# Kernel tuning notes

Hardware: AMD Instinct MI355X
Metric: run time of the kernel (lower is better)

Reference implementation:

```python
import jax, jax.numpy as jnp
import numpy as np

N_NODES = 100000
N_EDGES = 1600000
D_FEAT = 64
POS_DIM = 3
D_HID = 64


def setup_inputs() -> dict:
    key = jax.random.key(0)
    ks = jax.random.split(key, 8)
    s = lambda fan_in: 1.0 / np.sqrt(fan_in)
    x = jax.random.normal(ks[0], (N_NODES, D_FEAT), dtype=jnp.float32)
    pos = jax.random.normal(ks[1], (N_NODES, POS_DIM), dtype=jnp.float32)
    edge_index = jax.random.randint(ks[2], (2, N_EDGES), 0, N_NODES, dtype=jnp.int64)
    d_msg_in = 2 * D_FEAT + POS_DIM  # 131
    d_agg_in = 2 * D_FEAT            # 128
    return {
        "x": x,
        "edge_index": edge_index,
        "pos": pos,
        "mw1": jax.random.normal(ks[3], (d_msg_in, D_HID), dtype=jnp.float32) * s(d_msg_in),
        "mb1": jnp.zeros((D_HID,), dtype=jnp.float32),
        "mw2": jax.random.normal(ks[4], (D_HID, D_HID), dtype=jnp.float32) * s(D_HID),
        "mb2": jnp.zeros((D_HID,), dtype=jnp.float32),
        "aw1": jax.random.normal(ks[5], (d_agg_in, D_HID), dtype=jnp.float32) * s(d_agg_in),
        "ab1": jnp.zeros((D_HID,), dtype=jnp.float32),
        "aw2": jax.random.normal(ks[6], (D_HID, D_HID), dtype=jnp.float32) * s(D_HID),
        "ab2": jnp.zeros((D_HID,), dtype=jnp.float32),
    }


def reference(x, edge_index, pos, mw1, mb1, mw2, mb2, aw1, ab1, aw2, ab2):
    # flow='target_to_source': aggregation node i = edge_index[0], neighbor j = edge_index[1]
    i = edge_index[0]
    j = edge_index[1]
    # message: msg_net(cat[x_i, x_j, pos_j - pos_i])   [E, 2d+pos]
    inp = jnp.concatenate([x[i], x[j], pos[j] - pos[i]], axis=1)
    h = jax.nn.relu(inp @ mw1 + mb1)
    msg = h @ mw2 + mb2  # [E, D_HID]
    n = x.shape[0]
    # scatter-mean aggregate at node i
    msg_sum = jax.ops.segment_sum(msg, i, num_segments=n)
    cnt = jax.ops.segment_sum(jnp.ones((i.shape[0], 1), x.dtype), i, num_segments=n)
    aggr = msg_sum / jnp.maximum(cnt, 1.0)
    # update: aggr_net(cat[x, aggr])  (self_val=True)
    u = jnp.concatenate([x, aggr], axis=1)
    return jax.nn.relu(u @ aw1 + ab1) @ aw2 + ab2
```

## Files before the change

kernel.cpp:

```cpp
#include <hip/hip_runtime.h>
#include <hip/hip_fp16.h>

#define N_NODES 100000
#define N_EDGES 1600000
#define NPART 98
#define CAP   20480
#define EB    8192
#define NBB   ((N_EDGES + EB - 1) / EB)
#define NBT   ((N_NODES + 127) / 128)

typedef _Float16 half8 __attribute__((ext_vector_type(8)));
typedef float f32x4 __attribute__((ext_vector_type(4)));

#define WS_OFF   0
#define WS_PCUR  400016
#define WS_B     400528
#define WS_SJ    401040
#define WS_BCOMB 6817424
#define WS_PK    6817680
#define WS_Q     6858640
#define WS_BIN   19658640
#define WS_HM16  19658640

__global__ void __launch_bounds__(256) k_setup(const float* __restrict__ mw1,
                                               const float* __restrict__ mw2,
                                               const float* __restrict__ mb2,
                                               const float* __restrict__ aw1,
                                               const float* __restrict__ aw2,
                                               _Float16* __restrict__ pk,
                                               float* __restrict__ bcomb,
                                               int* __restrict__ pcur) {
    __shared__ float wc[4096];
    int blk = blockIdx.x, t = threadIdx.x;
    if (blk < 5) {
        const float* src;
        if (blk == 3) {
            for (int o = t; o < 4096; o += 256) {
                int c = o >> 6, k = o & 63;
                float s = 0.f;
                #pragma unroll 8
                for (int a = 0; a < 64; ++a) s += mw2[c * 64 + a] * aw1[(64 + a) * 64 + k];
                wc[o] = s;
            }
            __syncthreads();
            src = wc;
        } else {
            src = (blk == 0) ? mw1 : (blk == 1) ? (mw1 + 4096)
                : (blk == 2) ? aw1 : aw2;
        }
        _Float16* dst = pk + blk * 4096;
        for (int o = t; o < 4096; o += 256) {
            int b_ = o & 7, l = (o >> 3) & 63, z = o >> 9;
            int kg = z & 1, nt = z >> 1;
            int k = kg * 32 + ((l >> 4) << 3) + b_;
            int n = nt * 16 + (l & 15);
            dst[o] = (_Float16)src[k * 64 + n];
        }
    } else {
        if (t < 64) {
            float s = 0.f;
            #pragma unroll 8
            for (int a = 0; a < 64; ++a) s += mb2[a] * aw1[(64 + a) * 64 + t];
            bcomb[t] = s;
        }
        if (t < 128) pcur[t] = t * CAP;
    }
}

__device__ __forceinline__ half8 afrag_f32(const float* src, int row, int kg, int l) {
    const float* p = src + (size_t)row * 64 + kg * 32 + ((l >> 4) << 3);
    float4 u = *(const float4*)p;
    float4 v = *(const float4*)(p + 4);
    half8 h;
    h[0] = (_Float16)u.x; h[1] = (_Float16)u.y; h[2] = (_Float16)u.z; h[3] = (_Float16)u.w;
    h[4] = (_Float16)v.x; h[5] = (_Float16)v.y; h[6] = (_Float16)v.z; h[7] = (_Float16)v.w;
    return h;
}

__global__ void __launch_bounds__(256) k_binpre(const int* __restrict__ ei,
                                                const int* __restrict__ ej,
                                                int* pcur, int* __restrict__ binned,
                                                const float* __restrict__ x,
                                                const float* __restrict__ pos,
                                                const float* __restrict__ mw1,
                                                const float* __restrict__ mb1,
                                                const _Float16* __restrict__ pk,
                                                float* __restrict__ P,
                                                _Float16* __restrict__ Q16) {
    __shared__ int cnt[NPART];
    __shared__ int wcur[NPART];
    int t = threadIdx.x;
    if (blockIdx.x < NBB) {
        for (int q = t; q < NPART; q += 256) cnt[q] = 0;
        __syncthreads();
        int base_e = blockIdx.x * EB;
        #pragma unroll 2
        for (int it = 0; it < EB / 1024; ++it) {
            int e = base_e + it * 1024 + t * 4;
            if (e < N_EDGES) {
                int4 iv = *(const int4*)(ei + e);
                atomicAdd(&cnt[iv.x >> 10], 1);
                atomicAdd(&cnt[iv.y >> 10], 1);
                atomicAdd(&cnt[iv.z >> 10], 1);
                atomicAdd(&cnt[iv.w >> 10], 1);
            }
        }
        __syncthreads();
        for (int q = t; q < NPART; q += 256)
            wcur[q] = cnt[q] ? atomicAdd(&pcur[q], cnt[q]) : 0;
        __syncthreads();
        #pragma unroll 2
        for (int it = 0; it < EB / 1024; ++it) {
            int e = base_e + it * 1024 + t * 4;
            if (e < N_EDGES) {
                int4 iv = *(const int4*)(ei + e);
                int4 jv = *(const int4*)(ej + e);
                int a, p;
                p = iv.x >> 10; a = atomicAdd(&wcur[p], 1);
                if (a < (p + 1) * CAP) binned[a] = ((iv.x & 1023) << 17) | jv.x;
                p = iv.y >> 10; a = atomicAdd(&wcur[p], 1);
                if (a < (p + 1) * CAP) binned[a] = ((iv.y & 1023) << 17) | jv.y;
                p = iv.z >> 10; a = atomicAdd(&wcur[p], 1);
                if (a < (p + 1) * CAP) binned[a] = ((iv.z & 1023) << 17) | jv.z;
                p = iv.w >> 10; a = atomicAdd(&wcur[p], 1);
                if (a < (p + 1) * CAP) binned[a] = ((iv.w & 1023) << 17) | jv.w;
            }
        }
        return;
    }
    int bid = blockIdx.x - NBB;
    int w = t >> 6, l = t & 63;
    int m0 = bid * 128 + w * 32;

    half8 a[2][2];
    #pragma unroll
    for (int s = 0; s < 2; ++s)
        #pragma unroll
        for (int kg = 0; kg < 2; ++kg) {
            int row = m0 + s * 16 + (l & 15);
            if (row >= N_NODES) row = N_NODES - 1;
            a[s][kg] = afrag_f32(x, row, kg, l);
        }

    f32x4 z = {0.f, 0.f, 0.f, 0.f};
    f32x4 accP[2][4], accQ[2][4];
    #pragma unroll
    for (int s = 0; s < 2; ++s)
        #pragma unroll
        for (int nt = 0; nt < 4; ++nt) { accP[s][nt] = z; accQ[s][nt] = z; }

    #pragma unroll
    for (int nt = 0; nt < 4; ++nt)
        #pragma unroll
        for (int kg = 0; kg < 2; ++kg) {
            half8 b = *(const half8*)(pk + ((nt * 2 + kg) * 64 + l) * 8);
            accP[0][nt] = __builtin_amdgcn_mfma_f32_16x16x32_f16(a[0][kg], b, accP[0][nt], 0, 0, 0);
            accP[1][nt] = __builtin_amdgcn_mfma_f32_16x16x32_f16(a[1][kg], b, accP[1][nt], 0, 0, 0);
        }
    const _Float16* pkb = pk + 4096;
    #pragma unroll
    for (int nt = 0; nt < 4; ++nt)
        #pragma unroll
        for (int kg = 0; kg < 2; ++kg) {
            half8 b = *(const half8*)(pkb + ((nt * 2 + kg) * 64 + l) * 8);
            accQ[0][nt] = __builtin_amdgcn_mfma_f32_16x16x32_f16(a[0][kg], b, accQ[0][nt], 0, 0, 0);
            accQ[1][nt] = __builtin_amdgcn_mfma_f32_16x16x32_f16(a[1][kg], b, accQ[1][nt], 0, 0, 0);
        }

    int col = l & 15;
    float wx[4], wy[4], wz[4], bb[4];
    #pragma unroll
    for (int nt = 0; nt < 4; ++nt) {
        int n = nt * 16 + col;
        wx[nt] = mw1[128 * 64 + n];
        wy[nt] = mw1[129 * 64 + n];
        wz[nt] = mw1[130 * 64 + n];
        bb[nt] = mb1[n];
    }
    #pragma unroll
    for (int s = 0; s < 2; ++s)
        #pragma unroll
        for (int r = 0; r < 4; ++r) {
            int m = m0 + s * 16 + ((l >> 4) << 2) + r;
            if (m >= N_NODES) continue;
            float px = pos[3 * m], py = pos[3 * m + 1], pz = pos[3 * m + 2];
            #pragma unroll
            for (int nt = 0; nt < 4; ++nt) {
                int n = nt * 16 + col;
                float pd = px * wx[nt] + py * wy[nt] + pz * wz[nt];
                P[(size_t)m * 64 + n] = accP[s][nt][r] + bb[nt] - pd;
                Q16[(size_t)m * 64 + n] = (_Float16)(accQ[s][nt][r] + pd);
            }
        }
}

__global__ void __launch_bounds__(256) k_fill3s(const int* __restrict__ binned,
                                                const int* __restrict__ pcur,
                                                int* __restrict__ off,
                                                int* __restrict__ sj) {
    __shared__ int bs[128];
    __shared__ int hist[1024];
    __shared__ int tsum[256];
    int p = blockIdx.x, t = threadIdx.x;

    int c = 0;
    if (t < 128) {
        if (t < NPART) c = min(pcur[t] - t * CAP, CAP);
        bs[t] = c;
    }
    __syncthreads();
    for (int o = 1; o < 128; o <<= 1) {
        int a = 0;
        if (t < 128 && t >= o) a = bs[t - o];
        __syncthreads();
        if (t < 128) bs[t] += a;
        __syncthreads();
    }
    int cp = min(pcur[p] - p * CAP, CAP);
    int b0g = bs[p] - cp;
    int cnt_p = cp;
    int total = bs[NPART - 1];
    const int* src = binned + p * CAP;

    #pragma unroll
    for (int q = 0; q < 4; ++q) hist[t * 4 + q] = 0;
    __syncthreads();
    for (int e = t; e < cnt_p; e += 256) atomicAdd(&hist[src[e] >> 17], 1);
    __syncthreads();

    int b0 = hist[t * 4], b1 = hist[t * 4 + 1], b2 = hist[t * 4 + 2], b3 = hist[t * 4 + 3];
    int c1 = b0, c2 = c1 + b1, c3 = c2 + b2, tot = c3 + b3;
    tsum[t] = tot;
    __syncthreads();
    for (int o = 1; o < 256; o <<= 1) {
        int a = (t >= o) ? tsum[t - o] : 0;
        __syncthreads();
        tsum[t] += a;
        __syncthreads();
    }
    int tex = tsum[t] - tot;
    hist[t * 4]     = tex;
    hist[t * 4 + 1] = tex + c1;
    hist[t * 4 + 2] = tex + c2;
    hist[t * 4 + 3] = tex + c3;
    __syncthreads();

    int lo = p * 1024;
    #pragma unroll
    for (int q = 0; q < 4; ++q) {
        int n = t * 4 + q, g = lo + n;
        if (g < N_NODES) off[g] = b0g + hist[n];
    }
    if (p == NPART - 1 && t == 0) off[N_NODES] = total;
    __syncthreads();

    for (int e = t; e < cnt_p; e += 256) {
        int v = src[e];
        int slot = atomicAdd(&hist[v >> 17], 1);
        sj[b0g + slot] = v & 0x1FFFF;
    }
}

#define G1(k) int j##k = __builtin_amdgcn_readlane(jv, G + k); \
              float v##k = (float)Q16[(size_t)j##k * 64 + lane];
#define G2(k) r += (G + k < m) ? fmaxf(Pv + v##k, 0.f) : 0.f;

template<int G>
__device__ __forceinline__ float grp16(int jv, int m, float Pv, int lane,
                                       const _Float16* __restrict__ Q16) {
    if (G >= m) return 0.f;
    G1(0)  G1(1)  G1(2)  G1(3)  G1(4)  G1(5)  G1(6)  G1(7)
    G1(8)  G1(9)  G1(10) G1(11) G1(12) G1(13) G1(14) G1(15)
    float r = 0.f;
    G2(0)  G2(1)  G2(2)  G2(3)  G2(4)  G2(5)  G2(6)  G2(7)
    G2(8)  G2(9)  G2(10) G2(11) G2(12) G2(13) G2(14) G2(15)
    return r;
}

__global__ void __launch_bounds__(256) k_c1(const _Float16* __restrict__ Q16,
                                            const int* __restrict__ off,
                                            const int* __restrict__ sj,
                                            const float* __restrict__ Phm,
                                            _Float16* __restrict__ hm16) {
    int wave = threadIdx.x >> 6, lane = threadIdx.x & 63;
    int node = blockIdx.x * 4 + wave;
    if (node >= N_NODES) return;
    float Pv = __builtin_nontemporal_load(&Phm[(size_t)node * 64 + lane]);
    int o0 = off[node], o1 = off[node + 1];
    int dg = o1 - o0;
    float acc = 0.f;
    for (int base = o0; base < o1; base += 64) {
        int m = min(64, o1 - base);
        int jv = (lane < m) ? __builtin_nontemporal_load(&sj[base + lane]) : 0;
        acc += grp16<0>(jv, m, Pv, lane, Q16);
        acc += grp16<16>(jv, m, Pv, lane, Q16);
        acc += grp16<32>(jv, m, Pv, lane, Q16);
        acc += grp16<48>(jv, m, Pv, lane, Q16);
    }
    _Float16 hv = (_Float16)((dg > 0) ? acc / (float)dg : 0.f);
    __builtin_nontemporal_store(hv, &hm16[(size_t)node * 64 + lane]);
}

__global__ void __launch_bounds__(256) k_c2(const float* __restrict__ x,
                                            const _Float16* __restrict__ hm16,
                                            const _Float16* __restrict__ pk,
                                            const float* __restrict__ ab1,
                                            const float* __restrict__ bcomb,
                                            const float* __restrict__ ab2,
                                            const int* __restrict__ off,
                                            float* __restrict__ out) {
    __shared__ _Float16 lsh[4][2][16][64];
    int w = threadIdx.x >> 6, l = threadIdx.x & 63;
    int m0 = blockIdx.x * 128 + w * 32;
    int col = l & 15;

    f32x4 z = {0.f, 0.f, 0.f, 0.f};
    f32x4 acc[2][4];
    #pragma unroll
    for (int s = 0; s < 2; ++s)
        #pragma unroll
        for (int nt = 0; nt < 4; ++nt) acc[s][nt] = z;

    {
        half8 a[2][2];
        #pragma unroll
        for (int s = 0; s < 2; ++s)
            #pragma unroll
            for (int kg = 0; kg < 2; ++kg) {
                int row = m0 + s * 16 + (l & 15);
                if (row >= N_NODES) row = N_NODES - 1;
                a[s][kg] = afrag_f32(x, row, kg, l);
            }
        const _Float16* pk1 = pk + 2 * 4096;
        #pragma unroll
        for (int nt = 0; nt < 4; ++nt)
            #pragma unroll
            for (int kg = 0; kg < 2; ++kg) {
                half8 b = *(const half8*)(pk1 + ((nt * 2 + kg) * 64 + l) * 8);
                acc[0][nt] = __builtin_amdgcn_mfma_f32_16x16x32_f16(a[0][kg], b, acc[0][nt], 0, 0, 0);
                acc[1][nt] = __builtin_amdgcn_mfma_f32_16x16x32_f16(a[1][kg], b, acc[1][nt], 0, 0, 0);
            }
    }
    {
        half8 a[2][2];
        #pragma unroll
        for (int s = 0; s < 2; ++s)
            #pragma unroll
            for (int kg = 0; kg < 2; ++kg) {
                int row = m0 + s * 16 + (l & 15);
                if (row >= N_NODES) row = N_NODES - 1;
                a[s][kg] = *(const half8*)(hm16 + (size_t)row * 64 + kg * 32 + ((l >> 4) << 3));
            }
        const _Float16* pk2 = pk + 3 * 4096;
        #pragma unroll
        for (int nt = 0; nt < 4; ++nt)
            #pragma unroll
            for (int kg = 0; kg < 2; ++kg) {
                half8 b = *(const half8*)(pk2 + ((nt * 2 + kg) * 64 + l) * 8);
                acc[0][nt] = __builtin_amdgcn_mfma_f32_16x16x32_f16(a[0][kg], b, acc[0][nt], 0, 0, 0);
                acc[1][nt] = __builtin_amdgcn_mfma_f32_16x16x32_f16(a[1][kg], b, acc[1][nt], 0, 0, 0);
            }
    }

    float a1n[4], bcn[4];
    #pragma unroll
    for (int nt = 0; nt < 4; ++nt) {
        int n = nt * 16 + col;
        a1n[nt] = ab1[n];
        bcn[nt] = bcomb[n];
    }
    #pragma unroll
    for (int s = 0; s < 2; ++s)
        #pragma unroll
        for (int r = 0; r < 4; ++r) {
            int row = ((l >> 4) << 2) + r;
            int m = m0 + s * 16 + row;
            int dg = (m < N_NODES) ? (off[m + 1] - off[m]) : 0;
            #pragma unroll
            for (int nt = 0; nt < 4; ++nt) {
                int n = nt * 16 + col;
                float v = acc[s][nt][r] + a1n[nt] + ((dg > 0) ? bcn[nt] : 0.f);
                v = fmaxf(v, 0.f);
                lsh[w][s][row][n ^ ((row & 7) << 3)] = (_Float16)v;
            }
        }
    __syncthreads();

    f32x4 acc2[2][4];
    #pragma unroll
    for (int s = 0; s < 2; ++s)
        #pragma unroll
        for (int nt = 0; nt < 4; ++nt) acc2[s][nt] = z;
    {
        half8 a[2][2];
        #pragma unroll
        for (int s = 0; s < 2; ++s)
            #pragma unroll
            for (int kg = 0; kg < 2; ++kg) {
                int rr = l & 15;
                int c0 = (kg * 32 + ((l >> 4) << 3)) ^ ((rr & 7) << 3);
                a[s][kg] = *(const half8*)&lsh[w][s][rr][c0];
            }
        const _Float16* pk3 = pk + 4 * 4096;
        #pragma unroll
        for (int nt = 0; nt < 4; ++nt)
            #pragma unroll
            for (int kg = 0; kg < 2; ++kg) {
                half8 b = *(const half8*)(pk3 + ((nt * 2 + kg) * 64 + l) * 8);
                acc2[0][nt] = __builtin_amdgcn_mfma_f32_16x16x32_f16(a[0][kg], b, acc2[0][nt], 0, 0, 0);
                acc2[1][nt] = __builtin_amdgcn_mfma_f32_16x16x32_f16(a[1][kg], b, acc2[1][nt], 0, 0, 0);
            }
    }

    float a2n[4];
    #pragma unroll
    for (int nt = 0; nt < 4; ++nt) a2n[nt] = ab2[nt * 16 + col];
    #pragma unroll
    for (int s = 0; s < 2; ++s)
        #pragma unroll
        for (int r = 0; r < 4; ++r) {
            int m = m0 + s * 16 + ((l >> 4) << 2) + r;
            if (m >= N_NODES) continue;
            #pragma unroll
            for (int nt = 0; nt < 4; ++nt)
                out[(size_t)m * 64 + nt * 16 + col] = acc2[s][nt][r] + a2n[nt];
        }
}

extern "C" void kernel_launch(void* const* d_in, const int* in_sizes, int n_in,
                              void* d_out, int out_size, void* d_ws, size_t ws_size,
                              hipStream_t stream) {
    const float* x   = (const float*)d_in[0];
    const int*   ei  = (const int*)d_in[1];
    const int*   ej  = ((const int*)d_in[1]) + N_EDGES;
    const float* pos = (const float*)d_in[2];
    const float* mw1 = (const float*)d_in[3];
    const float* mb1 = (const float*)d_in[4];
    const float* mw2 = (const float*)d_in[5];
    const float* mb2 = (const float*)d_in[6];
    const float* aw1 = (const float*)d_in[7];
    const float* ab1 = (const float*)d_in[8];
    const float* aw2 = (const float*)d_in[9];
    const float* ab2 = (const float*)d_in[10];

    char* ws = (char*)d_ws;
    int*       off    = (int*)(ws + WS_OFF);
    int*       pcur   = (int*)(ws + WS_PCUR);
    int*       sj     = (int*)(ws + WS_SJ);
    float*     bcomb  = (float*)(ws + WS_BCOMB);
    _Float16*  pk     = (_Float16*)(ws + WS_PK);
    _Float16*  Q16    = (_Float16*)(ws + WS_Q);
    int*       binned = (int*)(ws + WS_BIN);
    _Float16*  hm16   = (_Float16*)(ws + WS_HM16);
    float*     out    = (float*)d_out;

    hipLaunchKernelGGL(k_setup,  dim3(6), dim3(256), 0, stream,
                       mw1, mw2, mb2, aw1, aw2, pk, bcomb, pcur);
    hipLaunchKernelGGL(k_binpre, dim3(NBB + NBT), dim3(256), 0, stream,
                       ei, ej, pcur, binned, x, pos, mw1, mb1, pk, out, Q16);
    hipLaunchKernelGGL(k_fill3s, dim3(NPART), dim3(256), 0, stream,
                       binned, pcur, off, sj);
    hipLaunchKernelGGL(k_c1,     dim3((N_NODES + 3) / 4), dim3(256), 0, stream,
                       Q16, off, sj, out, hm16);
    hipLaunchKernelGGL(k_c2,     dim3(NBT), dim3(256), 0, stream,
                       x, hm16, pk, ab1, bcomb, ab2, off, out);
}
```

Measured before the change: 162.4 us.

## Fuse edge aggregation and update MLP into one kernel via LDS

Merges the per-node gather/aggregate kernel with the update-MLP kernel. Each block aggregates its 128 nodes into a swizzled LDS tile and then runs the MFMA MLP on it. Degree flags are also kept in LDS. This removes the fp16 hidden buffer round trip through global memory and one launch. In exchange, the gather phase runs with far fewer blocks and waves, each wave serially processing 32 nodes, which reduces latency hiding for the random gathers.

```diff
diff --git a/kernel.cpp b/kernel.cpp
--- a/kernel.cpp
+++ b/kernel.cpp
@@ -14,13 +14,11 @@
 
 #define WS_OFF   0
 #define WS_PCUR  400016
-#define WS_B     400528
 #define WS_SJ    401040
 #define WS_BCOMB 6817424
 #define WS_PK    6817680
 #define WS_Q     6858640
 #define WS_BIN   19658640
-#define WS_HM16  19658640
 
 __global__ void __launch_bounds__(256) k_setup(const float* __restrict__ mw1,
                                                const float* __restrict__ mw2,
@@ -277,43 +275,49 @@
     return r;
 }
 
-__global__ void __launch_bounds__(256) k_c1(const _Float16* __restrict__ Q16,
-                                            const int* __restrict__ off,
-                                            const int* __restrict__ sj,
-                                            const float* __restrict__ Phm,
-                                            _Float16* __restrict__ hm16) {
+__global__ void __launch_bounds__(256) k_c12(const _Float16* __restrict__ Q16,
+                                             const int* __restrict__ off,
+                                             const int* __restrict__ sj,
+                                             const float* __restrict__ x,
+                                             const _Float16* __restrict__ pk,
+                                             const float* __restrict__ ab1,
+                                             const float* __restrict__ bcomb,
+                                             const float* __restrict__ ab2,
+                                             float* __restrict__ Pout) {
+    __shared__ _Float16 hm[128][64];
+    __shared__ _Float16 lsh[4][2][16][64];
+    __shared__ unsigned char flags[128];
     int wave = threadIdx.x >> 6, lane = threadIdx.x & 63;
-    int node = blockIdx.x * 4 + wave;
-    if (node >= N_NODES) return;
-    float Pv = __builtin_nontemporal_load(&Phm[(size_t)node * 64 + lane]);
-    int o0 = off[node], o1 = off[node + 1];
-    int dg = o1 - o0;
-    float acc = 0.f;
-    for (int base = o0; base < o1; base += 64) {
-        int m = min(64, o1 - base);
-        int jv = (lane < m) ? __builtin_nontemporal_load(&sj[base + lane]) : 0;
-        acc += grp16<0>(jv, m, Pv, lane, Q16);
-        acc += grp16<16>(jv, m, Pv, lane, Q16);
-        acc += grp16<32>(jv, m, Pv, lane, Q16);
-        acc += grp16<48>(jv, m, Pv, lane, Q16);
-    }
-    _Float16 hv = (_Float16)((dg > 0) ? acc / (float)dg : 0.f);
-    __builtin_nontemporal_store(hv, &hm16[(size_t)node * 64 + lane]);
-}
-
-__global__ void __launch_bounds__(256) k_c2(const float* __restrict__ x,
-                                            const _Float16* __restrict__ hm16,
-                                            const _Float16* __restrict__ pk,
-                                            const float* __restrict__ ab1,
-                                            const float* __restrict__ bcomb,
-                                            const float* __restrict__ ab2,
-                                            const int* __restrict__ off,
-                                            float* __restrict__ out) {
-    __shared__ _Float16 lsh[4][2][16][64];
-    int w = threadIdx.x >> 6, l = threadIdx.x & 63;
-    int m0 = blockIdx.x * 128 + w * 32;
+    int m0 = blockIdx.x * 128;
+
+    for (int n = wave; n < 128; n += 4) {
+        int node = m0 + n;
+        int sw = lane ^ ((n & 7) << 3);
+        if (node >= N_NODES) {
+            hm[n][sw] = (_Float16)0.f;
+            if (lane == 0) flags[n] = 0;
+            continue;
+        }
+        float Pv = __builtin_nontemporal_load(&Pout[(size_t)node * 64 + lane]);
+        int o0 = off[node], o1 = off[node + 1];
+        int dg = o1 - o0;
+        float acc = 0.f;
+        for (int base = o0; base < o1; base += 64) {
+            int m = min(64, o1 - base);
+            int jv = (lane < m) ? __builtin_nontemporal_load(&sj[base + lane]) : 0;
+            acc += grp16<0>(jv, m, Pv, lane, Q16);
+            acc += grp16<16>(jv, m, Pv, lane, Q16);
+            acc += grp16<32>(jv, m, Pv, lane, Q16);
+            acc += grp16<48>(jv, m, Pv, lane, Q16);
+        }
+        hm[n][sw] = (_Float16)((dg > 0) ? acc / (float)dg : 0.f);
+        if (lane == 0) flags[n] = (dg > 0) ? 1 : 0;
+    }
+    __syncthreads();
+
+    int w = wave, l = threadIdx.x & 63;
+    int mb = m0 + w * 32;
     int col = l & 15;
-
     f32x4 z = {0.f, 0.f, 0.f, 0.f};
     f32x4 acc[2][4];
     #pragma unroll
@@ -327,7 +331,7 @@
         for (int s = 0; s < 2; ++s)
             #pragma unroll
             for (int kg = 0; kg < 2; ++kg) {
-                int row = m0 + s * 16 + (l & 15);
+                int row = mb + s * 16 + (l & 15);
                 if (row >= N_NODES) row = N_NODES - 1;
                 a[s][kg] = afrag_f32(x, row, kg, l);
             }
@@ -347,9 +351,9 @@
         for (int s = 0; s < 2; ++s)
             #pragma unroll
             for (int kg = 0; kg < 2; ++kg) {
-                int row = m0 + s * 16 + (l & 15);
-                if (row >= N_NODES) row = N_NODES - 1;
-                a[s][kg] = *(const half8*)(hm16 + (size_t)row * 64 + kg * 32 + ((l >> 4) << 3));
+                int lr = w * 32 + s * 16 + (l & 15);
+                int c0 = (kg * 32 + ((l >> 4) << 3)) ^ ((lr & 7) << 3);
+                a[s][kg] = *(const half8*)&hm[lr][c0];
             }
         const _Float16* pk2 = pk + 3 * 4096;
         #pragma unroll
@@ -374,12 +378,12 @@
         #pragma unroll
         for (int r = 0; r < 4; ++r) {
             int row = ((l >> 4) << 2) + r;
-            int m = m0 + s * 16 + row;
-            int dg = (m < N_NODES) ? (off[m + 1] - off[m]) : 0;
+            int lr = w * 32 + s * 16 + row;
+            int fg = flags[lr];
             #pragma unroll
             for (int nt = 0; nt < 4; ++nt) {
                 int n = nt * 16 + col;
-                float v = acc[s][nt][r] + a1n[nt] + ((dg > 0) ? bcn[nt] : 0.f);
+                float v = acc[s][nt][r] + a1n[nt] + (fg ? bcn[nt] : 0.f);
                 v = fmaxf(v, 0.f);
                 lsh[w][s][row][n ^ ((row & 7) << 3)] = (_Float16)v;
             }
@@ -419,11 +423,11 @@
     for (int s = 0; s < 2; ++s)
         #pragma unroll
         for (int r = 0; r < 4; ++r) {
-            int m = m0 + s * 16 + ((l >> 4) << 2) + r;
+            int m = mb + s * 16 + ((l >> 4) << 2) + r;
             if (m >= N_NODES) continue;
             #pragma unroll
             for (int nt = 0; nt < 4; ++nt)
-                out[(size_t)m * 64 + nt * 16 + col] = acc2[s][nt][r] + a2n[nt];
+                Pout[(size_t)m * 64 + nt * 16 + col] = acc2[s][nt][r] + a2n[nt];
         }
 }
 
@@ -451,7 +455,6 @@
     _Float16*  pk     = (_Float16*)(ws + WS_PK);
     _Float16*  Q16    = (_Float16*)(ws + WS_Q);
     int*       binned = (int*)(ws + WS_BIN);
-    _Float16*  hm16   = (_Float16*)(ws + WS_HM16);
     float*     out    = (float*)d_out;
 
     hipLaunchKernelGGL(k_setup,  dim3(6), dim3(256), 0, stream,
@@ -460,8 +463,6 @@
                        ei, ej, pcur, binned, x, pos, mw1, mb1, pk, out, Q16);
     hipLaunchKernelGGL(k_fill3s, dim3(NPART), dim3(256), 0, stream,
                        binned, pcur, off, sj);
-    hipLaunchKernelGGL(k_c1,     dim3((N_NODES + 3) / 4), dim3(256), 0, stream,
-                       Q16, off, sj, out, hm16);
-    hipLaunchKernelGGL(k_c2,     dim3(NBT), dim3(256), 0, stream,
-                       x, hm16, pk, ab1, bcomb, ab2, off, out);
-}
+    hipLaunchKernelGGL(k_c12,    dim3(NBT), dim3(256), 0, stream,
+                       Q16, off, sj, x, pk, ab1, bcomb, ab2, out);
+}
```

Result: slower. 181.9 us (+12.0%).
